# Kernel tuning notes

Measured on AMD Instinct MI355X. Metric: run time of the kernel, lower is better.

Reference implementation:

```python
import jax, jax.numpy as jnp
import numpy as np

N = 50000
E = 600000
H = 128


def setup_inputs() -> dict:
    key = jax.random.key(0)
    ks = jax.random.split(key, 9)
    x = jax.random.normal(ks[0], (N, H), dtype=jnp.float32)
    edge_index = jax.random.randint(ks[1], (2, E), 0, N, dtype=jnp.int64)
    edge_weight = jax.random.uniform(ks[2], (E,), dtype=jnp.float32)
    s = 1.0 / np.sqrt(H)
    Wq = jax.random.normal(ks[3], (H, H), dtype=jnp.float32) * s
    bq = jnp.zeros((H,), dtype=jnp.float32)
    Wk = jax.random.normal(ks[4], (H, H), dtype=jnp.float32) * s
    bk = jnp.zeros((H,), dtype=jnp.float32)
    Wv = jax.random.normal(ks[5], (H, H), dtype=jnp.float32) * s
    bv = jnp.zeros((H,), dtype=jnp.float32)
    return {"x": x, "edge_index": edge_index, "edge_weight": edge_weight,
            "Wq": Wq, "bq": bq, "Wk": Wk, "bk": bk, "Wv": Wv, "bv": bv}


def reference(x, edge_index, edge_weight, Wq, bq, Wk, bk, Wv, bv):
    scale = jnp.sqrt(jnp.asarray(x.shape[-1], dtype=x.dtype))
    Q = x @ Wq.T + bq  # [N, H]
    K = x @ Wk.T + bk
    V = x @ Wv.T + bv
    row, col = edge_index[0], edge_index[1]  # [E]
    # per-edge scaled dot-product
    energy = jnp.sum(Q[row] * K[col], axis=-1) / scale  # [E]
    # NOTE: faithful to the source — softmax over ALL edges (dim=0), not per-node
    attn = jax.nn.softmax(energy * edge_weight, axis=0)  # [E]
    msgs = V[col] * attn[:, None]  # [E, H]
    out = jnp.zeros_like(x).at[row].add(msgs)  # scatter-add to destination nodes
    return out
```

## Files before the change

### kernel.cpp

```cpp
#include <hip/hip_runtime.h>
#include <hip/hip_bf16.h>

#define N_NODES 50000
#define E_EDGES 600000
#define HDIM    128

#define QKV_BLOCKS  ((N_NODES + 63) / 64)
#define EDGE_BLOCKS ((E_EDGES + 255) / 256)
#define SCAN_BLOCKS ((N_NODES + 255) / 256)
#define ROW_BLOCKS  (N_NODES / 4)

typedef float f32x4  __attribute__((ext_vector_type(4)));
typedef short short8 __attribute__((ext_vector_type(8)));

__device__ __forceinline__ unsigned short f2bf(float f) {
    __hip_bfloat16 h = __float2bfloat16(f);
    return *reinterpret_cast<unsigned short*>(&h);
}
__device__ __forceinline__ float bfdec(unsigned short s) {
    return __uint_as_float((unsigned)s << 16);
}
__device__ __forceinline__ float bflo(unsigned u) { return __uint_as_float(u << 16); }
__device__ __forceinline__ float bfhi(unsigned u) { return __uint_as_float(u & 0xffff0000u); }

__global__ __launch_bounds__(256) void qkv_hist_kernel(
    const float* __restrict__ x,
    const float* __restrict__ Wq, const float* __restrict__ bq,
    const float* __restrict__ Wk, const float* __restrict__ bk,
    const float* __restrict__ Wv, const float* __restrict__ bv,
    const int* __restrict__ ei, int* __restrict__ counts,
    float* __restrict__ Q, unsigned short* __restrict__ Kb,
    unsigned short* __restrict__ Vb)
{
    __shared__ __align__(16) unsigned short Ah[64 * HDIM];
    __shared__ __align__(16) unsigned short Al[64 * HDIM];
    const int bid = blockIdx.x;
    const int mat = bid / QKV_BLOCKS;
    const int r0  = (bid - mat * QKV_BLOCKS) * 64;

    for (int t = threadIdx.x; t < 2048; t += 256) {
        const int r  = t >> 5;
        const int k4 = t & 31;
        int gr = r0 + r; if (gr >= N_NODES) gr = N_NODES - 1;
        const float4 xv = *(const float4*)&x[(size_t)gr * HDIM + k4 * 4];
        ushort4 hv, lv;
        hv.x = f2bf(xv.x); hv.y = f2bf(xv.y);
        hv.z = f2bf(xv.z); hv.w = f2bf(xv.w);
        lv.x = f2bf(xv.x - bfdec(hv.x));
        lv.y = f2bf(xv.y - bfdec(hv.y));
        lv.z = f2bf(xv.z - bfdec(hv.z));
        lv.w = f2bf(xv.w - bfdec(hv.w));
        const int byte = (r << 8) + (k4 << 3);
        const int swz  = byte ^ ((r & 7) << 4);
        *(ushort4*)((char*)Ah + swz) = hv;
        *(ushort4*)((char*)Al + swz) = lv;
    }

    {
        const int e = bid * 256 + threadIdx.x;
        if (e < E_EDGES) atomicAdd(&counts[ei[e]], 1);
    }

    const int lane = threadIdx.x & 63;
    const int w    = threadIdx.x >> 6;
    const int lrow = lane & 15;
    const int lgrp = lane >> 4;
    const int nb   = w * 32;

    const float* Wm = (mat == 0) ? Wq : (mat == 1) ? Wk : Wv;
    const float* bm = (mat == 0) ? bq : (mat == 1) ? bk : bv;
    const float bias0 = bm[nb + lrow];
    const float bias1 = bm[nb + 16 + lrow];

    if (mat == 0) {
        short8 Bh[2][4], Bl[2][4];
#pragma unroll
        for (int st = 0; st < 2; ++st) {
            const int col = nb + st * 16 + lrow;
#pragma unroll
            for (int ks = 0; ks < 4; ++ks) {
                const int k0 = ks * 32 + lgrp * 8;
                const float* p = Wm + (size_t)col * HDIM + k0;
                const float4 a = *(const float4*)p;
                const float4 b = *(const float4*)(p + 4);
                const float f[8] = {a.x, a.y, a.z, a.w, b.x, b.y, b.z, b.w};
                short8 h, l;
#pragma unroll
                for (int j = 0; j < 8; ++j) {
                    h[j] = (short)f2bf(f[j]);
                    l[j] = (short)f2bf(f[j] - bfdec((unsigned short)h[j]));
                }
                Bh[st][ks] = h; Bl[st][ks] = l;
            }
        }
        __syncthreads();
#pragma unroll
        for (int s = 0; s < 4; ++s) {
            f32x4 acc0 = {0.f, 0.f, 0.f, 0.f};
            f32x4 acc1 = {0.f, 0.f, 0.f, 0.f};
            const int row = s * 16 + lrow;
#pragma unroll
            for (int ks = 0; ks < 4; ++ks) {
                const int byte = (row << 8) + ((ks * 32 + lgrp * 8) << 1);
                const int swz  = byte ^ ((row & 7) << 4);
                const short8 ah = *(const short8*)((const char*)Ah + swz);
                const short8 al = *(const short8*)((const char*)Al + swz);
                acc0 = __builtin_amdgcn_mfma_f32_16x16x32_bf16(ah, Bh[0][ks], acc0, 0, 0, 0);
                acc0 = __builtin_amdgcn_mfma_f32_16x16x32_bf16(al, Bh[0][ks], acc0, 0, 0, 0);
                acc0 = __builtin_amdgcn_mfma_f32_16x16x32_bf16(ah, Bl[0][ks], acc0, 0, 0, 0);
                acc1 = __builtin_amdgcn_mfma_f32_16x16x32_bf16(ah, Bh[1][ks], acc1, 0, 0, 0);
                acc1 = __builtin_amdgcn_mfma_f32_16x16x32_bf16(al, Bh[1][ks], acc1, 0, 0, 0);
                acc1 = __builtin_amdgcn_mfma_f32_16x16x32_bf16(ah, Bl[1][ks], acc1, 0, 0, 0);
            }
            const int orow0 = r0 + s * 16 + lgrp * 4;
#pragma unroll
            for (int i = 0; i < 4; ++i) {
                const int row_o = orow0 + i;
                if (row_o < N_NODES) {
                    Q[(size_t)row_o * HDIM + nb + lrow]      = acc0[i] + bias0;
                    Q[(size_t)row_o * HDIM + nb + 16 + lrow] = acc1[i] + bias1;
                }
            }
        }
    } else {
        short8 Bh[2][4];
#pragma unroll
        for (int st = 0; st < 2; ++st) {
            const int col = nb + st * 16 + lrow;
#pragma unroll
            for (int ks = 0; ks < 4; ++ks) {
                const int k0 = ks * 32 + lgrp * 8;
                const float* p = Wm + (size_t)col * HDIM + k0;
                const float4 a = *(const float4*)p;
                const float4 b = *(const float4*)(p + 4);
                const float f[8] = {a.x, a.y, a.z, a.w, b.x, b.y, b.z, b.w};
                short8 h;
#pragma unroll
                for (int j = 0; j < 8; ++j) h[j] = (short)f2bf(f[j]);
                Bh[st][ks] = h;
            }
        }
        __syncthreads();
        unsigned short* dst = (mat == 1) ? Kb : Vb;
#pragma unroll
        for (int s = 0; s < 4; ++s) {
            f32x4 acc0 = {0.f, 0.f, 0.f, 0.f};
            f32x4 acc1 = {0.f, 0.f, 0.f, 0.f};
            const int row = s * 16 + lrow;
#pragma unroll
            for (int ks = 0; ks < 4; ++ks) {
                const int byte = (row << 8) + ((ks * 32 + lgrp * 8) << 1);
                const int swz  = byte ^ ((row & 7) << 4);
                const short8 ah = *(const short8*)((const char*)Ah + swz);
                acc0 = __builtin_amdgcn_mfma_f32_16x16x32_bf16(ah, Bh[0][ks], acc0, 0, 0, 0);
                acc1 = __builtin_amdgcn_mfma_f32_16x16x32_bf16(ah, Bh[1][ks], acc1, 0, 0, 0);
            }
            const int orow0 = r0 + s * 16 + lgrp * 4;
#pragma unroll
            for (int i = 0; i < 4; ++i) {
                const int row_o = orow0 + i;
                if (row_o < N_NODES) {
                    dst[(size_t)row_o * HDIM + nb + lrow]      = f2bf(acc0[i] + bias0);
                    dst[(size_t)row_o * HDIM + nb + 16 + lrow] = f2bf(acc1[i] + bias1);
                }
            }
        }
    }
}

__global__ __launch_bounds__(256) void scan_partial_kernel(
    const int* __restrict__ counts, int* __restrict__ offs, int* __restrict__ aux)
{
    __shared__ int s[256];
    const int i = blockIdx.x * 256 + threadIdx.x;
    const int v = (i < N_NODES) ? counts[i] : 0;
    s[threadIdx.x] = v;
    __syncthreads();
    for (int d = 1; d < 256; d <<= 1) {
        int t = (threadIdx.x >= d) ? s[threadIdx.x - d] : 0;
        __syncthreads();
        s[threadIdx.x] += t;
        __syncthreads();
    }
    if (i < N_NODES) offs[i] = s[threadIdx.x] - v;
    if (threadIdx.x == 255) aux[blockIdx.x] = s[255];
}

__global__ __launch_bounds__(256) void scan_aux_kernel(int* __restrict__ aux)
{
    __shared__ int s[256];
    const int i = threadIdx.x;
    const int v = (i < SCAN_BLOCKS) ? aux[i] : 0;
    s[i] = v;
    __syncthreads();
    for (int d = 1; d < 256; d <<= 1) {
        int t = (i >= d) ? s[i - d] : 0;
        __syncthreads();
        s[i] += t;
        __syncthreads();
    }
    if (i < SCAN_BLOCKS) aux[i] = s[i] - v;
}

__global__ __launch_bounds__(256) void scan_add_kernel(
    int* __restrict__ offs, const int* __restrict__ aux, int* __restrict__ cursor)
{
    const int i = blockIdx.x * 256 + threadIdx.x;
    if (i < N_NODES) {
        const int o = offs[i] + aux[blockIdx.x];
        offs[i] = o;
        cursor[i] = o;
    }
}

__global__ __launch_bounds__(256) void bin_kernel(
    const int* __restrict__ ei, const float* __restrict__ ew,
    int* __restrict__ cursor, unsigned* __restrict__ pk)
{
    const int e = blockIdx.x * 256 + threadIdx.x;
    if (e >= E_EDGES) return;
    const int row = ei[e];
    const int pos = atomicAdd(&cursor[row], 1);
    const unsigned q = (unsigned)(ew[e] * 32767.f + 0.5f);
    pk[pos] = (unsigned)ei[E_EDGES + e] | (q << 17);
}

__global__ __launch_bounds__(256) void energy_kernel(
    const float* __restrict__ Q, const unsigned short* __restrict__ Kb,
    const int* __restrict__ offs, const int* __restrict__ counts,
    const unsigned* __restrict__ pk, float* __restrict__ p_arr,
    float* __restrict__ blocksum)
{
    const int row  = (blockIdx.x * 256 + threadIdx.x) >> 6;
    const int lane = threadIdx.x & 63;
    const int eg   = lane >> 4;
    const int sl   = lane & 15;
    const int start = offs[row], len = counts[row];
    const float4 q0 = *(const float4*)&Q[(size_t)row * HDIM + sl * 8];
    const float4 q1 = *(const float4*)&Q[(size_t)row * HDIM + sl * 8 + 4];
    const uint4* kb128 = (const uint4*)Kb;
    const float inv_scale = 0.08838834764831845f;
    const float dq = 1.0f / 32767.0f;
    float psum = 0.f;
    for (int j0 = 0; j0 < len; j0 += 16) {
        int e[4]; bool v[4]; unsigned r[4]; uint4 u[4];
#pragma unroll
        for (int c = 0; c < 4; ++c) {
            const int jj = j0 + c * 4 + eg;
            v[c] = jj < len;
            e[c] = start + (v[c] ? jj : 0);
            r[c] = pk[e[c]];
        }
#pragma unroll
        for (int c = 0; c < 4; ++c)
            u[c] = kb128[(size_t)(r[c] & 0x1FFFFu) * 16 + sl];
#pragma unroll
        for (int c = 0; c < 4; ++c) {
            float d = q0.x * bflo(u[c].x) + q0.y * bfhi(u[c].x)
                    + q0.z * bflo(u[c].y) + q0.w * bfhi(u[c].y)
                    + q1.x * bflo(u[c].z) + q1.y * bfhi(u[c].z)
                    + q1.z * bflo(u[c].w) + q1.w * bfhi(u[c].w);
#pragma unroll
            for (int m = 8; m >= 1; m >>= 1) d += __shfl_xor(d, m);
            const float ewv = (float)(r[c] >> 17) * dq;
            const float p = __expf(d * inv_scale * ewv);
            if (v[c] && sl == 0) { p_arr[e[c]] = p; psum += p; }
        }
    }
    psum += __shfl_xor(psum, 16);
    psum += __shfl_xor(psum, 32);
    __shared__ float sm[4];
    if (lane == 0) sm[threadIdx.x >> 6] = psum;
    __syncthreads();
    if (threadIdx.x == 0)
        blocksum[blockIdx.x] = sm[0] + sm[1] + sm[2] + sm[3];
}

__global__ __launch_bounds__(256) void reduce_sum_kernel(
    const float* __restrict__ bs, int n, float* __restrict__ gsum)
{
    float v = 0.f;
    for (int i = threadIdx.x; i < n; i += 256) v += bs[i];
#pragma unroll
    for (int s = 32; s >= 1; s >>= 1) v += __shfl_xor(v, s);
    __shared__ float sm[4];
    if ((threadIdx.x & 63) == 0) sm[threadIdx.x >> 6] = v;
    __syncthreads();
    if (threadIdx.x == 0) *gsum = sm[0] + sm[1] + sm[2] + sm[3];
}

__global__ __launch_bounds__(256) void accum_kernel(
    const unsigned short* __restrict__ Vb,
    const int* __restrict__ offs, const int* __restrict__ counts,
    const unsigned* __restrict__ pk, const float* __restrict__ p_arr,
    const float* __restrict__ gsum, float* __restrict__ out)
{
    const int row  = (blockIdx.x * 256 + threadIdx.x) >> 6;
    const int lane = threadIdx.x & 63;
    const int eg   = lane >> 4;
    const int sl   = lane & 15;
    const float inv = 1.0f / *gsum;
    const int start = offs[row], len = counts[row];
    const uint4* vb128 = (const uint4*)Vb;
    float acc[4][8];
#pragma unroll
    for (int c = 0; c < 4; ++c)
#pragma unroll
        for (int k = 0; k < 8; ++k) acc[c][k] = 0.f;
    for (int j0 = 0; j0 < len; j0 += 16) {
        unsigned r[4]; float w[4]; uint4 u[4];
#pragma unroll
        for (int c = 0; c < 4; ++c) {
            const int jj = j0 + c * 4 + eg;
            const bool v = jj < len;
            const int  e = start + (v ? jj : 0);
            r[c] = pk[e];
            w[c] = v ? p_arr[e] * inv : 0.f;
        }
#pragma unroll
        for (int c = 0; c < 4; ++c)
            u[c] = vb128[(size_t)(r[c] & 0x1FFFFu) * 16 + sl];
#pragma unroll
        for (int c = 0; c < 4; ++c) {
            acc[c][0] += bflo(u[c].x) * w[c];
            acc[c][1] += bfhi(u[c].x) * w[c];
            acc[c][2] += bflo(u[c].y) * w[c];
            acc[c][3] += bfhi(u[c].y) * w[c];
            acc[c][4] += bflo(u[c].z) * w[c];
            acc[c][5] += bfhi(u[c].z) * w[c];
            acc[c][6] += bflo(u[c].w) * w[c];
            acc[c][7] += bfhi(u[c].w) * w[c];
        }
    }
    float a[8];
#pragma unroll
    for (int k = 0; k < 8; ++k) {
        a[k] = (acc[0][k] + acc[1][k]) + (acc[2][k] + acc[3][k]);
        a[k] += __shfl_xor(a[k], 16);
        a[k] += __shfl_xor(a[k], 32);
    }
    if (eg == 0) {
        float* o = out + (size_t)row * HDIM + sl * 8;
        *(float4*)o       = make_float4(a[0], a[1], a[2], a[3]);
        *(float4*)(o + 4) = make_float4(a[4], a[5], a[6], a[7]);
    }
}

extern "C" void kernel_launch(void* const* d_in, const int* in_sizes, int n_in,
                              void* d_out, int out_size, void* d_ws, size_t ws_size,
                              hipStream_t stream)
{
    const float* x  = (const float*)d_in[0];
    const int*   ei = (const int*)d_in[1];
    const float* ew = (const float*)d_in[2];
    const float* Wq = (const float*)d_in[3];
    const float* bq = (const float*)d_in[4];
    const float* Wk = (const float*)d_in[5];
    const float* bk = (const float*)d_in[6];
    const float* Wv = (const float*)d_in[7];
    const float* bv = (const float*)d_in[8];
    float* out = (float*)d_out;

    float* ws = (float*)d_ws;
    float* Q       = ws;
    unsigned short* Kb = (unsigned short*)(Q + (size_t)N_NODES * HDIM);
    unsigned short* Vb = Kb + (size_t)N_NODES * HDIM;
    int*   counts  = (int*)(Vb + (size_t)N_NODES * HDIM);
    int*   offs    = counts + N_NODES;
    int*   cursor  = offs + N_NODES;
    int*   aux     = cursor + N_NODES;
    unsigned* pk   = (unsigned*)(aux + 256);
    float* p_arr   = (float*)(pk + E_EDGES);
    float* blocksum= p_arr + E_EDGES;
    float* gsum    = blocksum + ROW_BLOCKS;

    hipMemsetAsync(counts, 0, N_NODES * sizeof(int), stream);

    qkv_hist_kernel<<<3 * QKV_BLOCKS, 256, 0, stream>>>(
        x, Wq, bq, Wk, bk, Wv, bv, ei, counts, Q, Kb, Vb);
    scan_partial_kernel<<<SCAN_BLOCKS, 256, 0, stream>>>(counts, offs, aux);
    scan_aux_kernel<<<1, 256, 0, stream>>>(aux);
    scan_add_kernel<<<SCAN_BLOCKS, 256, 0, stream>>>(offs, aux, cursor);
    bin_kernel<<<EDGE_BLOCKS, 256, 0, stream>>>(ei, ew, cursor, pk);
    energy_kernel<<<ROW_BLOCKS, 256, 0, stream>>>(Q, Kb, offs, counts, pk, p_arr, blocksum);
    reduce_sum_kernel<<<1, 256, 0, stream>>>(blocksum, ROW_BLOCKS, gsum);
    accum_kernel<<<ROW_BLOCKS, 256, 0, stream>>>(Vb, offs, counts, pk, p_arr, gsum, out);
}
```

Before: 171.7 us.

## Split QKV kernel into Q+histogram and shared-tile K/V kernels

Replaces the single three-way QKV launch with a Q kernel that also builds the edge histogram and a separate K/V kernel that converts each x tile to bf16 once and reuses it for both K and V projections. This is meant to cut redundant x loads and conversions and shrink the grid. In exchange it adds a kernel launch and gives fewer blocks per stage, with serialized K then V work per block.

```diff
diff --git a/kernel.cpp b/kernel.cpp
--- a/kernel.cpp
+++ b/kernel.cpp
@@ -23,20 +23,16 @@
 __device__ __forceinline__ float bflo(unsigned u) { return __uint_as_float(u << 16); }
 __device__ __forceinline__ float bfhi(unsigned u) { return __uint_as_float(u & 0xffff0000u); }
 
-__global__ __launch_bounds__(256) void qkv_hist_kernel(
+__global__ __launch_bounds__(256) void qkv_q_kernel(
     const float* __restrict__ x,
     const float* __restrict__ Wq, const float* __restrict__ bq,
-    const float* __restrict__ Wk, const float* __restrict__ bk,
-    const float* __restrict__ Wv, const float* __restrict__ bv,
     const int* __restrict__ ei, int* __restrict__ counts,
-    float* __restrict__ Q, unsigned short* __restrict__ Kb,
-    unsigned short* __restrict__ Vb)
+    float* __restrict__ Q)
 {
     __shared__ __align__(16) unsigned short Ah[64 * HDIM];
     __shared__ __align__(16) unsigned short Al[64 * HDIM];
     const int bid = blockIdx.x;
-    const int mat = bid / QKV_BLOCKS;
-    const int r0  = (bid - mat * QKV_BLOCKS) * 64;
+    const int r0  = bid * 64;
 
     for (int t = threadIdx.x; t < 2048; t += 256) {
         const int r  = t >> 5;
@@ -56,8 +52,9 @@
         *(ushort4*)((char*)Al + swz) = lv;
     }
 
-    {
-        const int e = bid * 256 + threadIdx.x;
+#pragma unroll
+    for (int c = 0; c < 3; ++c) {
+        const int e = bid * 768 + c * 256 + threadIdx.x;
         if (e < E_EDGES) atomicAdd(&counts[ei[e]], 1);
     }
 
@@ -67,62 +64,96 @@
     const int lgrp = lane >> 4;
     const int nb   = w * 32;
 
-    const float* Wm = (mat == 0) ? Wq : (mat == 1) ? Wk : Wv;
-    const float* bm = (mat == 0) ? bq : (mat == 1) ? bk : bv;
-    const float bias0 = bm[nb + lrow];
-    const float bias1 = bm[nb + 16 + lrow];
-
-    if (mat == 0) {
-        short8 Bh[2][4], Bl[2][4];
-#pragma unroll
-        for (int st = 0; st < 2; ++st) {
-            const int col = nb + st * 16 + lrow;
-#pragma unroll
-            for (int ks = 0; ks < 4; ++ks) {
-                const int k0 = ks * 32 + lgrp * 8;
-                const float* p = Wm + (size_t)col * HDIM + k0;
-                const float4 a = *(const float4*)p;
-                const float4 b = *(const float4*)(p + 4);
-                const float f[8] = {a.x, a.y, a.z, a.w, b.x, b.y, b.z, b.w};
-                short8 h, l;
-#pragma unroll
-                for (int j = 0; j < 8; ++j) {
-                    h[j] = (short)f2bf(f[j]);
-                    l[j] = (short)f2bf(f[j] - bfdec((unsigned short)h[j]));
-                }
-                Bh[st][ks] = h; Bl[st][ks] = l;
+    short8 Bh[2][4], Bl[2][4];
+#pragma unroll
+    for (int st = 0; st < 2; ++st) {
+        const int col = nb + st * 16 + lrow;
+#pragma unroll
+        for (int ks = 0; ks < 4; ++ks) {
+            const int k0 = ks * 32 + lgrp * 8;
+            const float* p = Wq + (size_t)col * HDIM + k0;
+            const float4 a = *(const float4*)p;
+            const float4 b = *(const float4*)(p + 4);
+            const float f[8] = {a.x, a.y, a.z, a.w, b.x, b.y, b.z, b.w};
+            short8 h, l;
+#pragma unroll
+            for (int j = 0; j < 8; ++j) {
+                h[j] = (short)f2bf(f[j]);
+                l[j] = (short)f2bf(f[j] - bfdec((unsigned short)h[j]));
             }
-        }
-        __syncthreads();
-#pragma unroll
-        for (int s = 0; s < 4; ++s) {
-            f32x4 acc0 = {0.f, 0.f, 0.f, 0.f};
-            f32x4 acc1 = {0.f, 0.f, 0.f, 0.f};
-            const int row = s * 16 + lrow;
-#pragma unroll
-            for (int ks = 0; ks < 4; ++ks) {
-                const int byte = (row << 8) + ((ks * 32 + lgrp * 8) << 1);
-                const int swz  = byte ^ ((row & 7) << 4);
-                const short8 ah = *(const short8*)((const char*)Ah + swz);
-                const short8 al = *(const short8*)((const char*)Al + swz);
-                acc0 = __builtin_amdgcn_mfma_f32_16x16x32_bf16(ah, Bh[0][ks], acc0, 0, 0, 0);
-                acc0 = __builtin_amdgcn_mfma_f32_16x16x32_bf16(al, Bh[0][ks], acc0, 0, 0, 0);
-                acc0 = __builtin_amdgcn_mfma_f32_16x16x32_bf16(ah, Bl[0][ks], acc0, 0, 0, 0);
-                acc1 = __builtin_amdgcn_mfma_f32_16x16x32_bf16(ah, Bh[1][ks], acc1, 0, 0, 0);
-                acc1 = __builtin_amdgcn_mfma_f32_16x16x32_bf16(al, Bh[1][ks], acc1, 0, 0, 0);
-                acc1 = __builtin_amdgcn_mfma_f32_16x16x32_bf16(ah, Bl[1][ks], acc1, 0, 0, 0);
+            Bh[st][ks] = h; Bl[st][ks] = l;
+        }
+    }
+    const float bias0 = bq[nb + lrow];
+    const float bias1 = bq[nb + 16 + lrow];
+
+    __syncthreads();
+
+#pragma unroll
+    for (int s = 0; s < 4; ++s) {
+        f32x4 acc0 = {0.f, 0.f, 0.f, 0.f};
+        f32x4 acc1 = {0.f, 0.f, 0.f, 0.f};
+        const int row = s * 16 + lrow;
+#pragma unroll
+        for (int ks = 0; ks < 4; ++ks) {
+            const int byte = (row << 8) + ((ks * 32 + lgrp * 8) << 1);
+            const int swz  = byte ^ ((row & 7) << 4);
+            const short8 ah = *(const short8*)((const char*)Ah + swz);
+            const short8 al = *(const short8*)((const char*)Al + swz);
+            acc0 = __builtin_amdgcn_mfma_f32_16x16x32_bf16(ah, Bh[0][ks], acc0, 0, 0, 0);
+            acc0 = __builtin_amdgcn_mfma_f32_16x16x32_bf16(al, Bh[0][ks], acc0, 0, 0, 0);
+            acc0 = __builtin_amdgcn_mfma_f32_16x16x32_bf16(ah, Bl[0][ks], acc0, 0, 0, 0);
+            acc1 = __builtin_amdgcn_mfma_f32_16x16x32_bf16(ah, Bh[1][ks], acc1, 0, 0, 0);
+            acc1 = __builtin_amdgcn_mfma_f32_16x16x32_bf16(al, Bh[1][ks], acc1, 0, 0, 0);
+            acc1 = __builtin_amdgcn_mfma_f32_16x16x32_bf16(ah, Bl[1][ks], acc1, 0, 0, 0);
+        }
+        const int orow0 = r0 + s * 16 + lgrp * 4;
+#pragma unroll
+        for (int i = 0; i < 4; ++i) {
+            const int row_o = orow0 + i;
+            if (row_o < N_NODES) {
+                Q[(size_t)row_o * HDIM + nb + lrow]      = acc0[i] + bias0;
+                Q[(size_t)row_o * HDIM + nb + 16 + lrow] = acc1[i] + bias1;
             }
-            const int orow0 = r0 + s * 16 + lgrp * 4;
-#pragma unroll
-            for (int i = 0; i < 4; ++i) {
-                const int row_o = orow0 + i;
-                if (row_o < N_NODES) {
-                    Q[(size_t)row_o * HDIM + nb + lrow]      = acc0[i] + bias0;
-                    Q[(size_t)row_o * HDIM + nb + 16 + lrow] = acc1[i] + bias1;
-                }
-            }
-        }
-    } else {
+        }
+    }
+}
+
+__global__ __launch_bounds__(256) void kv_kernel(
+    const float* __restrict__ x,
+    const float* __restrict__ Wk, const float* __restrict__ bk,
+    const float* __restrict__ Wv, const float* __restrict__ bv,
+    unsigned short* __restrict__ Kb, unsigned short* __restrict__ Vb)
+{
+    __shared__ __align__(16) unsigned short Ah[64 * HDIM];
+    const int r0 = blockIdx.x * 64;
+
+    for (int t = threadIdx.x; t < 2048; t += 256) {
+        const int r  = t >> 5;
+        const int k4 = t & 31;
+        int gr = r0 + r; if (gr >= N_NODES) gr = N_NODES - 1;
+        const float4 xv = *(const float4*)&x[(size_t)gr * HDIM + k4 * 4];
+        ushort4 hv;
+        hv.x = f2bf(xv.x); hv.y = f2bf(xv.y);
+        hv.z = f2bf(xv.z); hv.w = f2bf(xv.w);
+        const int byte = (r << 8) + (k4 << 3);
+        const int swz  = byte ^ ((r & 7) << 4);
+        *(ushort4*)((char*)Ah + swz) = hv;
+    }
+    __syncthreads();
+
+    const int lane = threadIdx.x & 63;
+    const int w    = threadIdx.x >> 6;
+    const int lrow = lane & 15;
+    const int lgrp = lane >> 4;
+    const int nb   = w * 32;
+
+#pragma unroll 1
+    for (int mat = 0; mat < 2; ++mat) {
+        const float* Wm = mat ? Wv : Wk;
+        const float* bm = mat ? bv : bk;
+        unsigned short* dst = mat ? Vb : Kb;
+
         short8 Bh[2][4];
 #pragma unroll
         for (int st = 0; st < 2; ++st) {
@@ -140,8 +171,9 @@
                 Bh[st][ks] = h;
             }
         }
-        __syncthreads();
-        unsigned short* dst = (mat == 1) ? Kb : Vb;
+        const float bias0 = bm[nb + lrow];
+        const float bias1 = bm[nb + 16 + lrow];
+
 #pragma unroll
         for (int s = 0; s < 4; ++s) {
             f32x4 acc0 = {0.f, 0.f, 0.f, 0.f};
@@ -376,8 +408,8 @@
 
     hipMemsetAsync(counts, 0, N_NODES * sizeof(int), stream);
 
-    qkv_hist_kernel<<<3 * QKV_BLOCKS, 256, 0, stream>>>(
-        x, Wq, bq, Wk, bk, Wv, bv, ei, counts, Q, Kb, Vb);
+    qkv_q_kernel<<<QKV_BLOCKS, 256, 0, stream>>>(x, Wq, bq, ei, counts, Q);
+    kv_kernel<<<QKV_BLOCKS, 256, 0, stream>>>(x, Wk, bk, Wv, bv, Kb, Vb);
     scan_partial_kernel<<<SCAN_BLOCKS, 256, 0, stream>>>(counts, offs, aux);
     scan_aux_kernel<<<1, 256, 0, stream>>>(aux);
     scan_add_kernel<<<SCAN_BLOCKS, 256, 0, stream>>>(offs, aux, cursor);
```

Result: slower. 195.0 us (+13.6%).
